# Kernel tuning notes

Hardware: AMD Instinct MI355X
Metric: run time of the kernel (lower is better)

## Reference

```python
import jax, jax.numpy as jnp
import numpy as np

D_MODEL = 1024
NHEAD = 16
HEAD_DIM = D_MODEL // NHEAD
EPS = 1e-5


def layernorm(x, g, b):
    mu = jnp.mean(x, axis=-1, keepdims=True)
    var = jnp.mean(jnp.square(x - mu), axis=-1, keepdims=True)
    return (x - mu) * jax.lax.rsqrt(var + EPS) * g + b


def setup_inputs() -> dict:
    key = jax.random.key(0)
    ks = jax.random.split(key, 10)
    B, S, D = 8, 2048, D_MODEL
    s = 1.0 / np.sqrt(D)
    return {
        "x": jax.random.normal(ks[0], (B, S, D), dtype=jnp.float32),
        "wq": jax.random.normal(ks[1], (D, D), dtype=jnp.float32) * s,
        "wk": jax.random.normal(ks[2], (D, D), dtype=jnp.float32) * s,
        "wv": jax.random.normal(ks[3], (D, D), dtype=jnp.float32) * s,
        "ln1_g": jnp.ones((D,), dtype=jnp.float32),
        "ln1_b": jnp.zeros((D,), dtype=jnp.float32),
        "ln2_g": jnp.ones((D,), dtype=jnp.float32),
        "ln2_b": jnp.zeros((D,), dtype=jnp.float32),
        "w1": jax.random.normal(ks[4], (D, D), dtype=jnp.float32) * s,
        "b1": jnp.zeros((D,), dtype=jnp.float32),
        "w2": jax.random.normal(ks[5], (D, D), dtype=jnp.float32) * s,
        "b2": jnp.zeros((D,), dtype=jnp.float32),
    }


def reference(x, wq, wk, wv, ln1_g, ln1_b, ln2_g, ln2_b, w1, b1, w2, b2):
    B, S, D = x.shape
    H, Dh = NHEAD, HEAD_DIM
    xn = layernorm(x, ln1_g, ln1_b)
    # nn.Linear: y = x @ W.T (no bias for q/k/v)
    q = (xn @ wq.T).reshape(B, S, H, Dh)
    k = (xn @ wk.T).reshape(B, S, H, Dh)
    v = (xn @ wv.T).reshape(B, S, H, Dh)
    scale = 1.0 / jnp.sqrt(jnp.float32(Dh))
    scores = jnp.einsum("bqhd,bkhd->bhqk", q, k) * scale  # [B,H,S,S]
    attn = jax.nn.softmax(scores, axis=-1)
    att = jnp.einsum("bhqk,bkhd->bqhd", attn, v).reshape(B, S, D)
    xt = layernorm(xn + att, ln2_g, ln2_b)
    ffn = jax.nn.relu(xt @ w1.T + b1) @ w2.T + b2
    return xt + ffn
```

## Files before the change

### kernel.cpp

```cpp
#include <hip/hip_runtime.h>
#include <hip/hip_bf16.h>

typedef __bf16 bf16x8 __attribute__((ext_vector_type(8)));
typedef float f32x4 __attribute__((ext_vector_type(4)));
typedef float f32x16 __attribute__((ext_vector_type(16)));

#define MFMA_B16(a, b, c) __builtin_amdgcn_mfma_f32_16x16x32_bf16((a), (b), (c), 0, 0, 0)
#define MFMA32_B16(a, b, c) __builtin_amdgcn_mfma_f32_32x32x16_bf16((a), (b), (c), 0, 0, 0)
#define GLD16(g, l)                                                              \
    __builtin_amdgcn_global_load_lds((__attribute__((address_space(1))) void*)(g), \
                                     (__attribute__((address_space(3))) void*)(l), \
                                     16, 0, 0)

__device__ __forceinline__ float bfu2f(unsigned short u) {
    return __uint_as_float(((unsigned)u) << 16);
}
__device__ __forceinline__ unsigned short f2bfu(float f) {
    unsigned u = __float_as_uint(f);
    u += 0x7fffu + ((u >> 16) & 1u);
    return (unsigned short)(u >> 16);
}
__device__ __forceinline__ float fexp2(float x) {
#if __has_builtin(__builtin_amdgcn_exp2f)
    return __builtin_amdgcn_exp2f(x);
#else
    return __expf(x * 0.69314718f);
#endif
}
__device__ __forceinline__ unsigned cvtpk_bf16(float lo_, float hi_) {
    unsigned r;
    asm("v_cvt_pk_bf16_f32 %0, %1, %2" : "=v"(r) : "v"(lo_), "v"(hi_));
    return r;
}
__device__ __forceinline__ void plswap(unsigned& a, unsigned& b) {
#if __has_builtin(__builtin_amdgcn_permlane32_swap)
    typedef int v2i __attribute__((ext_vector_type(2)));
    v2i r = __builtin_amdgcn_permlane32_swap((int)a, (int)b, false, false);
    a = (unsigned)r.x;
    b = (unsigned)r.y;
#else
    unsigned pa_ = (unsigned)__shfl_xor((int)a, 32);
    unsigned pb_ = (unsigned)__shfl_xor((int)b, 32);
    bool hi = (threadIdx.x & 63) >= 32;
    unsigned na = hi ? pb_ : a;
    unsigned nb = hi ? b : pa_;
    a = na;
    b = nb;
#endif
}

__global__ __launch_bounds__(256) void cvt5_f32_bf16(const float* __restrict__ s0,
                                                     const float* __restrict__ s1,
                                                     const float* __restrict__ s2,
                                                     const float* __restrict__ s3,
                                                     const float* __restrict__ s4,
                                                     unsigned short* __restrict__ dst) {
    int wsel = blockIdx.x >> 10;
    int i = (blockIdx.x & 1023) * 256 + threadIdx.x;
    const float* src = s0;
    if (wsel == 1) src = s1;
    else if (wsel == 2) src = s2;
    else if (wsel == 3) src = s3;
    else if (wsel == 4) src = s4;
    float4 v = ((const float4*)src)[i];
    ((ushort4*)dst)[wsel * 262144 + i] =
        make_ushort4(f2bfu(v.x), f2bfu(v.y), f2bfu(v.z), f2bfu(v.w));
}

__global__ __launch_bounds__(256) void ln1_kernel(const float* __restrict__ in1,
                                                  const float* __restrict__ gam,
                                                  const float* __restrict__ bet,
                                                  unsigned short* __restrict__ outb) {
    int row = blockIdx.x, tid = threadIdx.x;
    size_t base = (size_t)row * 1024 + tid * 4;
    float4 v = *(const float4*)(in1 + base);
    float s = v.x + v.y + v.z + v.w;
    float sq = v.x * v.x + v.y * v.y + v.z * v.z + v.w * v.w;
#pragma unroll
    for (int m = 1; m < 64; m <<= 1) {
        s += __shfl_xor(s, m);
        sq += __shfl_xor(sq, m);
    }
    __shared__ float red[8];
    int w = tid >> 6;
    if ((tid & 63) == 0) { red[w] = s; red[w + 4] = sq; }
    __syncthreads();
    s = red[0] + red[1] + red[2] + red[3];
    sq = red[4] + red[5] + red[6] + red[7];
    float mean = s * (1.0f / 1024.0f);
    float var = fmaxf(sq * (1.0f / 1024.0f) - mean * mean, 0.0f);
    float rstd = rsqrtf(var + 1e-5f);
    float4 g4 = *(const float4*)(gam + tid * 4);
    float4 b4 = *(const float4*)(bet + tid * 4);
    *(ushort4*)(outb + base) = make_ushort4(
        f2bfu((v.x - mean) * rstd * g4.x + b4.x), f2bfu((v.y - mean) * rstd * g4.y + b4.y),
        f2bfu((v.z - mean) * rstd * g4.z + b4.z), f2bfu((v.w - mean) * rstd * g4.w + b4.w));
}

__global__ __launch_bounds__(256) void ln2_kernel(const unsigned short* __restrict__ in1,
                                                  const unsigned short* __restrict__ in2,
                                                  const float* __restrict__ gam,
                                                  const float* __restrict__ bet,
                                                  unsigned short* __restrict__ outb) {
    int row = blockIdx.x, tid = threadIdx.x;
    size_t base = (size_t)row * 1024 + tid * 4;
    ushort4 a = *(const ushort4*)(in1 + base);
    ushort4 c = *(const ushort4*)(in2 + base);
    float4 v = make_float4(bfu2f(a.x) + bfu2f(c.x), bfu2f(a.y) + bfu2f(c.y),
                           bfu2f(a.z) + bfu2f(c.z), bfu2f(a.w) + bfu2f(c.w));
    float s = v.x + v.y + v.z + v.w;
    float sq = v.x * v.x + v.y * v.y + v.z * v.z + v.w * v.w;
#pragma unroll
    for (int m = 1; m < 64; m <<= 1) {
        s += __shfl_xor(s, m);
        sq += __shfl_xor(sq, m);
    }
    __shared__ float red[8];
    int w = tid >> 6;
    if ((tid & 63) == 0) { red[w] = s; red[w + 4] = sq; }
    __syncthreads();
    s = red[0] + red[1] + red[2] + red[3];
    sq = red[4] + red[5] + red[6] + red[7];
    float mean = s * (1.0f / 1024.0f);
    float var = fmaxf(sq * (1.0f / 1024.0f) - mean * mean, 0.0f);
    float rstd = rsqrtf(var + 1e-5f);
    float4 g4 = *(const float4*)(gam + tid * 4);
    float4 b4 = *(const float4*)(bet + tid * 4);
    *(ushort4*)(outb + base) = make_ushort4(
        f2bfu((v.x - mean) * rstd * g4.x + b4.x), f2bfu((v.y - mean) * rstd * g4.y + b4.y),
        f2bfu((v.z - mean) * rstd * g4.z + b4.z), f2bfu((v.w - mean) * rstd * g4.w + b4.w));
}

template <int MODE>
__global__ __launch_bounds__(512, 2) void gemm3(const unsigned short* __restrict__ A,
                                                const unsigned short* __restrict__ Bw,
                                                const float* __restrict__ bias,
                                                const unsigned short* __restrict__ resid,
                                                void* __restrict__ O0,
                                                void* __restrict__ O1,
                                                void* __restrict__ O2,
                                                int M, int N, int K) {
    __shared__ unsigned short As[3][256 * 64];
    __shared__ unsigned short Bs[3][128 * 64];
    int nt = N >> 7;
    int bid = blockIdx.x;
    int nwg = gridDim.x;
    int swz = (bid & 7) * (nwg >> 3) + (bid >> 3);
    int mt = swz / nt, ntl = swz % nt;
    int mbase = mt << 8, nbase = ntl << 7;
    int tid = threadIdx.x;
    int w = tid >> 6, l = tid & 63;
    int wm = w >> 2, wn = w & 3;
    int lr = l & 15, lg = l >> 4;

    int srow = tid >> 3;
    int csrc = (tid & 7) ^ (srow & 7);
    const unsigned short* ag = A + (size_t)(mbase + srow) * K + csrc * 8;
    const unsigned short* bg = Bw + (size_t)(nbase + srow) * K + csrc * 8;

    auto stage = [&](int t) {
        int buf = t % 3;
        const unsigned short* a = ag + (size_t)t * 64;
        const unsigned short* b = bg + (size_t)t * 64;
#pragma unroll
        for (int j = 0; j < 4; j++)
            GLD16(a + (size_t)j * 64 * K, &As[buf][j * 4096 + w * 512]);
#pragma unroll
        for (int j = 0; j < 2; j++)
            GLD16(b + (size_t)j * 64 * K, &Bs[buf][j * 4096 + w * 512]);
    };

    f32x4 acc[8][2] = {};
    int NT = K >> 6;

    stage(0);
    stage(1);
    asm volatile("s_waitcnt vmcnt(6)" ::: "memory");
    __builtin_amdgcn_s_barrier();

    for (int t = 0; t < NT; t++) {
        int buf = t % 3;
        if (t + 2 < NT) stage(t + 2);
        const unsigned short* Ab = &As[buf][(wm * 128) * 64];
        const unsigned short* Bb = &Bs[buf][(wn * 32) * 64];
#pragma unroll
        for (int ks = 0; ks < 2; ks++) {
            bf16x8 af[8], bf[2];
#pragma unroll
            for (int m = 0; m < 8; m++)
                af[m] = *(const bf16x8*)(Ab + (m * 16 + lr) * 64 +
                                         (((ks * 4 + lg) ^ (lr & 7)) << 3));
#pragma unroll
            for (int n = 0; n < 2; n++)
                bf[n] = *(const bf16x8*)(Bb + (n * 16 + lr) * 64 +
                                         (((ks * 4 + lg) ^ (lr & 7)) << 3));
            __builtin_amdgcn_s_setprio(1);
#pragma unroll
            for (int m = 0; m < 8; m++)
#pragma unroll
                for (int n = 0; n < 2; n++)
                    acc[m][n] = MFMA_B16(af[m], bf[n], acc[m][n]);
            __builtin_amdgcn_s_setprio(0);
        }
        if (t < NT - 1) {
            if (t + 2 < NT) asm volatile("s_waitcnt vmcnt(6)" ::: "memory");
            else asm volatile("s_waitcnt vmcnt(0)" ::: "memory");
            __builtin_amdgcn_s_barrier();
        }
    }

#pragma unroll
    for (int m = 0; m < 8; m++) {
        int row = mbase + wm * 128 + m * 16 + lg * 4;
#pragma unroll
        for (int n = 0; n < 2; n++) {
            int col = nbase + wn * 32 + n * 16 + lr;
            if constexpr (MODE == 0) {
                int wsel = col >> 10;
                int cl = col & 1023;
                if (wsel == 2) {
                    int hh = cl >> 6, dd = cl & 63;
                    int bb = row >> 11, ss = row & 2047;
                    unsigned short t4[4];
#pragma unroll
                    for (int j = 0; j < 4; j++) t4[j] = f2bfu(acc[m][n][j]);
                    size_t vtidx = ((size_t)((bb * 16 + hh) * 64 + dd)) * 2048 + ss;
                    *(uint2*)((unsigned short*)O2 + vtidx) = *(uint2*)t4;
                } else {
                    unsigned short* out = (wsel == 0) ? (unsigned short*)O0 : (unsigned short*)O1;
                    float sc = (wsel == 0) ? 0.18033688f : 1.0f;
#pragma unroll
                    for (int j = 0; j < 4; j++)
                        out[(size_t)(row + j) * 1024 + cl] = f2bfu(acc[m][n][j] * sc);
                }
            } else {
                float bv = bias[col];
#pragma unroll
                for (int j = 0; j < 4; j++) {
                    float v = acc[m][n][j] + bv;
                    size_t idx = (size_t)(row + j) * N + col;
                    if constexpr (MODE == 1) {
                        ((unsigned short*)O0)[idx] = f2bfu(fmaxf(v, 0.0f));
                    } else {
                        ((float*)O0)[idx] = v + bfu2f(resid[idx]);
                    }
                }
            }
        }
    }
}

__global__ __launch_bounds__(512) void attn_kernel(const unsigned short* __restrict__ qq,
                                                   const unsigned short* __restrict__ kk,
                                                   const unsigned short* __restrict__ vT,
                                                   unsigned short* __restrict__ attb) {
    __shared__ unsigned short Ks[2][64 * 64];
    __shared__ unsigned short Vs[2][64 * 64];

    int bid = blockIdx.x;
    int swz = (bid & 7) * (gridDim.x >> 3) + (bid >> 3);
    int qi = swz & 7, h = (swz >> 3) & 15, b = swz >> 7;
    int tid = threadIdx.x, w = tid >> 6, l = tid & 63;
    int lo = l & 31, hi = l >> 5;
    int q0 = qi * 256 + w * 32;

    const unsigned short* qp = qq + ((size_t)((b * 2048 + q0 + lo) * 16 + h)) * 64 + hi * 8;
    bf16x8 qf[4];
#pragma unroll
    for (int kc = 0; kc < 4; kc++) qf[kc] = *(const bf16x8*)(qp + kc * 16);

    int srow = w * 8 + (l >> 3);
    int schunk = (l & 7) ^ ((l >> 3) & 7);
    const unsigned short* ksrc = kk + ((size_t)((b * 2048 + srow) * 16 + h)) * 64 + schunk * 8;
    const unsigned short* vsrc = vT + ((size_t)((b * 16 + h) * 64 + srow)) * 2048 + schunk * 8;

    f32x16 od0 = {}, od1 = {};
    float ssum = 0.f;

    GLD16(ksrc, &Ks[0][w * 512]);
    GLD16(vsrc, &Vs[0][w * 512]);
    ksrc += 65536;
    vsrc += 64;
    asm volatile("s_waitcnt vmcnt(0)");
    __syncthreads();

    int cur = 0;
    for (int t = 0; t < 32; t++) {
        if (t < 31) {
            GLD16(ksrc, &Ks[cur ^ 1][w * 512]);
            GLD16(vsrc, &Vs[cur ^ 1][w * 512]);
            ksrc += 65536;
            vsrc += 64;
        }
        const unsigned short* Kb = &Ks[cur][0];
        f32x16 sacc[2];
        __builtin_amdgcn_s_setprio(1);
#pragma unroll
        for (int tt = 0; tt < 2; tt++) {
            f32x16 s = {};
            int row = tt * 32 + lo;
#pragma unroll
            for (int kc = 0; kc < 4; kc++) {
                bf16x8 a = *(const bf16x8*)(Kb + row * 64 + (((kc * 2 + hi) ^ (row & 7)) << 3));
                s = MFMA32_B16(a, qf[kc], s);
            }
            sacc[tt] = s;
        }
        __builtin_amdgcn_s_setprio(0);
        float p[32];
        float psum = 0.f;
#pragma unroll
        for (int tt = 0; tt < 2; tt++)
#pragma unroll
            for (int r = 0; r < 16; r++) {
                float e = fexp2(sacc[tt][r]);
                p[tt * 16 + r] = e;
                psum += e;
            }
        psum += __shfl_xor(psum, 32);
        ssum += psum;
        const unsigned short* Vb = &Vs[cur][0];
#pragma unroll
        for (int tt = 0; tt < 2; tt++) {
            unsigned wv[8];
#pragma unroll
            for (int i = 0; i < 8; i++) wv[i] = cvtpk_bf16(p[tt * 16 + 2 * i], p[tt * 16 + 2 * i + 1]);
            plswap(wv[0], wv[2]);
            plswap(wv[1], wv[3]);
            plswap(wv[4], wv[6]);
            plswap(wv[5], wv[7]);
            union { unsigned u[4]; bf16x8 v; } c0, c1;
            c0.u[0] = wv[0]; c0.u[1] = wv[1]; c0.u[2] = wv[2]; c0.u[3] = wv[3];
            c1.u[0] = wv[4]; c1.u[1] = wv[5]; c1.u[2] = wv[6]; c1.u[3] = wv[7];
            __builtin_amdgcn_s_setprio(1);
#pragma unroll
            for (int sub = 0; sub < 2; sub++) {
                int ks = tt * 2 + sub;
                bf16x8 pa = sub ? c1.v : c0.v;
                int slot = ((ks * 2 + hi) ^ (lo & 7)) << 3;
                bf16x8 v0 = *(const bf16x8*)(Vb + lo * 64 + slot);
                bf16x8 v1 = *(const bf16x8*)(Vb + (32 + lo) * 64 + slot);
                od0 = MFMA32_B16(pa, v0, od0);
                od1 = MFMA32_B16(pa, v1, od1);
            }
            __builtin_amdgcn_s_setprio(0);
        }
        asm volatile("s_waitcnt vmcnt(0)");
        __syncthreads();
        cur ^= 1;
    }

#pragma unroll
    for (int r = 0; r < 16; r++) {
        int crow = (r & 3) + ((r >> 2) << 3) + (hi << 2);
        float rs = 1.0f / __shfl(ssum, crow);
        int q = q0 + crow;
        size_t base = ((size_t)((b * 2048 + q) * 16 + h)) * 64;
        attb[base + lo] = f2bfu(od0[r] * rs);
        attb[base + 32 + lo] = f2bfu(od1[r] * rs);
    }
}

extern "C" void kernel_launch(void* const* d_in, const int* in_sizes, int n_in,
                              void* d_out, int out_size, void* d_ws, size_t ws_size,
                              hipStream_t stream) {
    const float* x = (const float*)d_in[0];
    const float* wq = (const float*)d_in[1];
    const float* wk = (const float*)d_in[2];
    const float* wv = (const float*)d_in[3];
    const float* ln1_g = (const float*)d_in[4];
    const float* ln1_b = (const float*)d_in[5];
    const float* ln2_g = (const float*)d_in[6];
    const float* ln2_b = (const float*)d_in[7];
    const float* w1 = (const float*)d_in[8];
    const float* b1 = (const float*)d_in[9];
    const float* w2 = (const float*)d_in[10];
    const float* b2 = (const float*)d_in[11];

    const size_t NB = 33554432;
    char* ws = (char*)d_ws;
    unsigned short* xn_b = (unsigned short*)(ws);
    unsigned short* q_b = (unsigned short*)(ws + NB);
    unsigned short* k_b = (unsigned short*)(ws + 2 * NB);
    unsigned short* vT_b = (unsigned short*)(ws + 3 * NB);
    unsigned short* att_b = (unsigned short*)(ws + 4 * NB);
    unsigned short* wq_b = (unsigned short*)(ws + 5 * NB);
    unsigned short* w1_b = wq_b + 3145728;
    unsigned short* w2_b = w1_b + 1048576;
    unsigned short* xt_b = q_b;
    unsigned short* h_b = k_b;

    dim3 blk(256);
    cvt5_f32_bf16<<<5120, blk, 0, stream>>>(wq, wk, wv, w1, w2, wq_b);
    ln1_kernel<<<16384, blk, 0, stream>>>(x, ln1_g, ln1_b, xn_b);

    gemm3<0><<<1536, dim3(512), 0, stream>>>(xn_b, wq_b, nullptr, nullptr,
                                             q_b, k_b, vT_b, 16384, 3072, 1024);

    attn_kernel<<<1024, dim3(512), 0, stream>>>(q_b, k_b, vT_b, att_b);

    ln2_kernel<<<16384, blk, 0, stream>>>(xn_b, att_b, ln2_g, ln2_b, xt_b);

    gemm3<1><<<512, dim3(512), 0, stream>>>(xt_b, w1_b, b1, nullptr,
                                            h_b, nullptr, nullptr, 16384, 1024, 1024);
    gemm3<2><<<512, dim3(512), 0, stream>>>(h_b, w2_b, b2, xt_b,
                                            d_out, nullptr, nullptr, 16384, 1024, 1024);
}
```

Measured before the change: 465.2 us.

## Enlarge GEMM tile to 256x256 with 8-phase interleaved load/MFMA ping-pong schedule

Replaces the 256x128 triple-buffered GEMM with a 256x256 tile kernel split into half-tiles. Each K-step is broken into eight phases that interleave LDS reads, global-to-LDS prefetch and MFMA clusters, with barriers between phases, so memory traffic overlaps with compute. The larger tile raises arithmetic intensity but halves the grid (768/256 blocks) and doubles the accumulator registers per thread, which may hurt occupancy and load balance across CUs. The many barriers and sched_barrier calls also add synchronisation overhead.

```diff
diff --git a/kernel.cpp b/kernel.cpp
--- a/kernel.cpp
+++ b/kernel.cpp
@@ -132,89 +132,118 @@
 }
 
 template <int MODE>
-__global__ __launch_bounds__(512, 2) void gemm3(const unsigned short* __restrict__ A,
+__global__ __launch_bounds__(512, 2) void gemm8(const unsigned short* __restrict__ A,
                                                 const unsigned short* __restrict__ Bw,
                                                 const float* __restrict__ bias,
                                                 const unsigned short* __restrict__ resid,
-                                                void* __restrict__ O0,
-                                                void* __restrict__ O1,
-                                                void* __restrict__ O2,
-                                                int M, int N, int K) {
-    __shared__ unsigned short As[3][256 * 64];
-    __shared__ unsigned short Bs[3][128 * 64];
-    int nt = N >> 7;
+                                                void* __restrict__ O0, void* __restrict__ O1,
+                                                void* __restrict__ O2, int M, int N, int K) {
+    __shared__ unsigned short As[4][8192];
+    __shared__ unsigned short Bs[4][8192];
+    int nt = N >> 8;
     int bid = blockIdx.x;
     int nwg = gridDim.x;
     int swz = (bid & 7) * (nwg >> 3) + (bid >> 3);
     int mt = swz / nt, ntl = swz % nt;
-    int mbase = mt << 8, nbase = ntl << 7;
+    int mbase = mt << 8, nbase = ntl << 8;
     int tid = threadIdx.x;
     int w = tid >> 6, l = tid & 63;
     int wm = w >> 2, wn = w & 3;
     int lr = l & 15, lg = l >> 4;
+    int lx = lr & 7;
+    int brow = (wn & 1) * 64;
 
     int srow = tid >> 3;
     int csrc = (tid & 7) ^ (srow & 7);
-    const unsigned short* ag = A + (size_t)(mbase + srow) * K + csrc * 8;
-    const unsigned short* bg = Bw + (size_t)(nbase + srow) * K + csrc * 8;
-
-    auto stage = [&](int t) {
-        int buf = t % 3;
-        const unsigned short* a = ag + (size_t)t * 64;
-        const unsigned short* b = bg + (size_t)t * 64;
-#pragma unroll
-        for (int j = 0; j < 4; j++)
-            GLD16(a + (size_t)j * 64 * K, &As[buf][j * 4096 + w * 512]);
-#pragma unroll
-        for (int j = 0; j < 2; j++)
-            GLD16(b + (size_t)j * 64 * K, &Bs[buf][j * 4096 + w * 512]);
+    const unsigned short* aRow = A + (size_t)(mbase + srow) * K + csrc * 8;
+    const unsigned short* bRow = Bw + (size_t)(nbase + srow) * K + csrc * 8;
+
+    const int NT = K >> 6;
+    auto stA = [&](int buf, int h, int t) {
+        if (t >= NT) return;
+        const unsigned short* s0 = aRow + (size_t)(h * 128) * K + t * 64;
+        GLD16(s0, &As[buf * 2 + h][w * 512]);
+        GLD16(s0 + (size_t)64 * K, &As[buf * 2 + h][4096 + w * 512]);
     };
-
-    f32x4 acc[8][2] = {};
-    int NT = K >> 6;
-
-    stage(0);
-    stage(1);
-    asm volatile("s_waitcnt vmcnt(6)" ::: "memory");
-    __builtin_amdgcn_s_barrier();
-
-    for (int t = 0; t < NT; t++) {
-        int buf = t % 3;
-        if (t + 2 < NT) stage(t + 2);
-        const unsigned short* Ab = &As[buf][(wm * 128) * 64];
-        const unsigned short* Bb = &Bs[buf][(wn * 32) * 64];
-#pragma unroll
-        for (int ks = 0; ks < 2; ks++) {
-            bf16x8 af[8], bf[2];
-#pragma unroll
-            for (int m = 0; m < 8; m++)
-                af[m] = *(const bf16x8*)(Ab + (m * 16 + lr) * 64 +
-                                         (((ks * 4 + lg) ^ (lr & 7)) << 3));
-#pragma unroll
-            for (int n = 0; n < 2; n++)
-                bf[n] = *(const bf16x8*)(Bb + (n * 16 + lr) * 64 +
-                                         (((ks * 4 + lg) ^ (lr & 7)) << 3));
-            __builtin_amdgcn_s_setprio(1);
-#pragma unroll
-            for (int m = 0; m < 8; m++)
-#pragma unroll
-                for (int n = 0; n < 2; n++)
-                    acc[m][n] = MFMA_B16(af[m], bf[n], acc[m][n]);
-            __builtin_amdgcn_s_setprio(0);
-        }
-        if (t < NT - 1) {
-            if (t + 2 < NT) asm volatile("s_waitcnt vmcnt(6)" ::: "memory");
-            else asm volatile("s_waitcnt vmcnt(0)" ::: "memory");
-            __builtin_amdgcn_s_barrier();
-        }
+    auto stB = [&](int buf, int h, int t) {
+        if (t >= NT) return;
+        const unsigned short* s0 = bRow + (size_t)(h * 128) * K + t * 64;
+        GLD16(s0, &Bs[buf * 2 + h][w * 512]);
+        GLD16(s0 + (size_t)64 * K, &Bs[buf * 2 + h][4096 + w * 512]);
+    };
+
+    f32x4 acc[8][4] = {};
+    bf16x8 afr[4][2], bq0[2][2], bq1[2][2];
+
+    auto rdA = [&](int buf, int mq) {
+        const unsigned short* base = &As[buf * 2 + wm][0];
+#pragma unroll
+        for (int mf = 0; mf < 4; mf++)
+#pragma unroll
+            for (int ks = 0; ks < 2; ks++)
+                afr[mf][ks] = *(const bf16x8*)(base + (mq * 64 + mf * 16 + lr) * 64 +
+                                               (((ks * 4 + lg) ^ lx) << 3));
+    };
+    auto rdB = [&](int buf, int nq, bf16x8 (&bf)[2][2]) {
+        const unsigned short* base = &Bs[buf * 2 + (wn >> 1)][0];
+#pragma unroll
+        for (int nf = 0; nf < 2; nf++)
+#pragma unroll
+            for (int ks = 0; ks < 2; ks++)
+                bf[nf][ks] = *(const bf16x8*)(base + (brow + nq * 32 + nf * 16 + lr) * 64 +
+                                              (((ks * 4 + lg) ^ lx) << 3));
+    };
+    auto MM = [&](int mq, int nq, bf16x8 (&bf)[2][2]) {
+        __builtin_amdgcn_s_setprio(1);
+#pragma unroll
+        for (int mf = 0; mf < 4; mf++)
+#pragma unroll
+            for (int nf = 0; nf < 2; nf++)
+#pragma unroll
+                for (int ks = 0; ks < 2; ks++)
+                    acc[mq * 4 + mf][nq * 2 + nf] =
+                        MFMA_B16(afr[mf][ks], bf[nf][ks], acc[mq * 4 + mf][nq * 2 + nf]);
+        __builtin_amdgcn_s_setprio(0);
+    };
+#define BARX __builtin_amdgcn_s_barrier()
+#define LGK0 do { asm volatile("s_waitcnt lgkmcnt(0)" ::: "memory"); \
+                  __builtin_amdgcn_sched_barrier(0); } while (0)
+#define VMC(n) asm volatile("s_waitcnt vmcnt(" #n ")" ::: "memory")
+
+    stA(0, 0, 0); stA(0, 1, 0); stB(0, 0, 0); stB(0, 1, 0); stB(1, 0, 1); stB(1, 1, 1);
+    VMC(4);
+    BARX;
+
+    int NIT = NT >> 1;
+    for (int i = 0; i < NIT; i++) {
+        int t0 = 2 * i, t1 = t0 + 1;
+        bool lastI = (i == NIT - 1);
+        rdA(0, 0); rdB(0, 0, bq0); stA(1, 0, t1);
+        BARX; LGK0; MM(0, 0, bq0); BARX;
+        rdB(0, 1, bq1); stA(1, 1, t1);
+        BARX; LGK0; MM(0, 1, bq1); BARX;
+        rdA(0, 1); stB(0, 0, t0 + 2);
+        BARX; LGK0; MM(1, 1, bq1); BARX;
+        stB(0, 1, t0 + 2);
+        if (lastI) { VMC(0); } else { VMC(4); }
+        BARX; MM(1, 0, bq0); BARX;
+        rdA(1, 0); rdB(1, 0, bq0); stA(0, 0, t0 + 2);
+        BARX; LGK0; MM(0, 0, bq0); BARX;
+        rdB(1, 1, bq1); stA(0, 1, t0 + 2);
+        BARX; LGK0; MM(0, 1, bq1); BARX;
+        rdA(1, 1); stB(1, 0, t1 + 2);
+        BARX; LGK0; MM(1, 1, bq1); BARX;
+        stB(1, 1, t1 + 2);
+        if (!lastI) { VMC(4); }
+        BARX; MM(1, 0, bq0); BARX;
     }
 
 #pragma unroll
     for (int m = 0; m < 8; m++) {
-        int row = mbase + wm * 128 + m * 16 + lg * 4;
-#pragma unroll
-        for (int n = 0; n < 2; n++) {
-            int col = nbase + wn * 32 + n * 16 + lr;
+        int row = mbase + wm * 128 + (m >> 2) * 64 + (m & 3) * 16 + lg * 4;
+#pragma unroll
+        for (int n = 0; n < 4; n++) {
+            int col = nbase + wn * 64 + (n >> 1) * 32 + (n & 1) * 16 + lr;
             if constexpr (MODE == 0) {
                 int wsel = col >> 10;
                 int cl = col & 1023;
@@ -248,6 +277,9 @@
             }
         }
     }
+#undef BARX
+#undef LGK0
+#undef VMC
 }
 
 __global__ __launch_bounds__(512) void attn_kernel(const unsigned short* __restrict__ qq,
@@ -394,15 +426,15 @@
     cvt5_f32_bf16<<<5120, blk, 0, stream>>>(wq, wk, wv, w1, w2, wq_b);
     ln1_kernel<<<16384, blk, 0, stream>>>(x, ln1_g, ln1_b, xn_b);
 
-    gemm3<0><<<1536, dim3(512), 0, stream>>>(xn_b, wq_b, nullptr, nullptr,
-                                             q_b, k_b, vT_b, 16384, 3072, 1024);
+    gemm8<0><<<768, dim3(512), 0, stream>>>(xn_b, wq_b, nullptr, nullptr,
+                                            q_b, k_b, vT_b, 16384, 3072, 1024);
 
     attn_kernel<<<1024, dim3(512), 0, stream>>>(q_b, k_b, vT_b, att_b);
 
     ln2_kernel<<<16384, blk, 0, stream>>>(xn_b, att_b, ln2_g, ln2_b, xt_b);
 
-    gemm3<1><<<512, dim3(512), 0, stream>>>(xt_b, w1_b, b1, nullptr,
+    gemm8<1><<<256, dim3(512), 0, stream>>>(xt_b, w1_b, b1, nullptr,
                                             h_b, nullptr, nullptr, 16384, 1024, 1024);
-    gemm3<2><<<512, dim3(512), 0, stream>>>(h_b, w2_b, b2, xt_b,
+    gemm8<2><<<256, dim3(512), 0, stream>>>(h_b, w2_b, b2, xt_b,
                                             d_out, nullptr, nullptr, 16384, 1024, 1024);
 }
```

New measurement: 394.6 us. 15.2% less time.
